# Performance work log

Measured on AMD Instinct MI355X. Metric: run time of the kernel, lower is better.

Reference implementation:

```python
import jax, jax.numpy as jnp
import numpy as np

NUM_CODES = 100000
NUM_EDGES = 20000
DIM = 128
DEG = 32  # nodes per hyperedge -> 640000 incidences


def setup_inputs() -> dict:
    key = jax.random.key(0)
    k1, k2, k3, k4, k5 = jax.random.split(key, 5)
    n_inc = NUM_EDGES * DEG
    # incidence list: edge_ids is sorted (CSR-style), node_ids are member nodes
    node_ids = jax.random.randint(k1, (n_inc,), 0, NUM_CODES, dtype=jnp.int32)
    edge_ids = jnp.repeat(jnp.arange(NUM_EDGES, dtype=jnp.int32), DEG)
    # learned parameters (xavier-ish scales)
    node_emb = jax.random.normal(k2, (NUM_CODES, DIM), jnp.float32) * (1.0 / np.sqrt(DIM))
    edge_emb = jax.random.normal(k3, (NUM_EDGES, DIM), jnp.float32) * (1.0 / np.sqrt(DIM))
    W_e = jax.random.normal(k4, (DIM, DIM), jnp.float32) * (1.0 / np.sqrt(DIM))
    b_e = jnp.zeros((DIM,), jnp.float32)
    W_v = jax.random.normal(k5, (DIM, DIM), jnp.float32) * (1.0 / np.sqrt(DIM))
    b_v = jnp.zeros((DIM,), jnp.float32)
    return {"node_emb": node_emb, "edge_emb": edge_emb, "W_e": W_e, "b_e": b_e,
            "W_v": W_v, "b_v": b_v, "node_ids": node_ids, "edge_ids": edge_ids}


def reference(node_emb, edge_emb, W_e, b_e, W_v, b_v, node_ids, edge_ids):
    N, D = node_emb.shape
    E = edge_emb.shape[0]
    # node -> edge: mean of member node embeddings per hyperedge (segment mean)
    gathered = node_emb[node_ids]                                    # [I, D]
    seg_sum = jax.ops.segment_sum(gathered, edge_ids, num_segments=E)  # [E, D]
    seg_cnt = jax.ops.segment_sum(jnp.ones_like(edge_ids, jnp.float32), edge_ids, num_segments=E)
    mean = seg_sum / jnp.maximum(seg_cnt, 1.0)[:, None]
    # empty edges fall back to their own edge embedding (as in the torch loop)
    edge_ctx = jnp.where(seg_cnt[:, None] > 0, mean, edge_emb)
    edge_ctx = edge_ctx @ W_e.T + b_e                                # lin_e
    # edge -> node: scatter-add edge_ctx back to member nodes
    node_sum = jnp.zeros_like(node_emb).at[node_ids].add(edge_ctx[edge_ids])
    deg = jnp.zeros((N,), jnp.float32).at[node_ids].add(1.0)
    node_cnt = 1.0 + deg  # torch code clamps zeros to 1 BEFORE adding counts
    node_ctx = (node_sum / node_cnt[:, None]) @ W_v.T + b_v          # lin_v
    node_out = node_emb + node_ctx
    edge_out = edge_emb + edge_ctx
    return (node_out, edge_out)
```

## Files before the change

### kernel.cpp

```cpp
#include <hip/hip_runtime.h>

#define DIMS 128
#define DEG 32
#define CAP 32

typedef __attribute__((ext_vector_type(8))) short short8;
typedef __attribute__((ext_vector_type(4))) float floatx4;

static __device__ __forceinline__ unsigned short f2bf(float f) {
  unsigned int u = __float_as_uint(f);
  unsigned int r = (u + 0x7FFFu + ((u >> 16) & 1u)) >> 16;
  return (unsigned short)r;
}
static __device__ __forceinline__ float bf2f(unsigned short v) {
  return __uint_as_float(((unsigned int)v) << 16);
}

__global__ __launch_bounds__(256) void k_cvt_all(
    const float* __restrict__ a0, unsigned short* __restrict__ d0, int n0,
    const float* __restrict__ a1, unsigned short* __restrict__ d1, int n1,
    int* __restrict__ cnt, int ncnt) {
  int t = blockIdx.x * 256 + threadIdx.x;
  if (t < ncnt) cnt[t] = 0;
  int i = t * 4;
  const float* s; unsigned short* d;
  if (i < n0) { s = a0 + i; d = d0 + i; }
  else if (i < n0 + n1) { s = a1 + (i - n0); d = d1 + (i - n0); }
  else return;
  float4 v = *(const float4*)s;
  ushort4 o;
  o.x = f2bf(v.x); o.y = f2bf(v.y); o.z = f2bf(v.z); o.w = f2bf(v.w);
  *(ushort4*)d = o;
}

__global__ __launch_bounds__(256) void k_prep_wc(
    const float* __restrict__ Wv, const float* __restrict__ We,
    const float* __restrict__ be,
    unsigned short* __restrict__ Wc, float* __restrict__ bc) {
  int tid = threadIdx.x;
  if (blockIdx.x == 16) {
    __shared__ float be_s[DIMS];
    if (tid < DIMS) be_s[tid] = be[tid];
    __syncthreads();
    if (tid < DIMS) {
      float s = 0.f;
      for (int c = 0; c < DIMS; ++c) s += Wv[(size_t)tid * DIMS + c] * be_s[c];
      bc[tid] = s;
    }
    return;
  }
  __shared__ __align__(16) float We_s[DIMS][DIMS];
  __shared__ __align__(16) float wv_s[8][DIMS];
  int d0 = blockIdx.x * 8;
#pragma unroll
  for (int u = 0; u < 16; ++u) {
    int idx = tid + u * 256;
    int row = idx >> 5, c4 = idx & 31;
    *(float4*)&We_s[row][c4 * 4] = ((const float4*)We)[idx];
  }
  {
    int row = tid >> 5, c4 = tid & 31;
    *(float4*)&wv_s[row][c4 * 4] = ((const float4*)(Wv + (size_t)d0 * DIMS))[tid];
  }
  __syncthreads();
  int dd = tid >> 5;
  int k4 = (tid & 31) * 4;
  float4 acc = {0.f, 0.f, 0.f, 0.f};
  for (int c = 0; c < DIMS; ++c) {
    float w = wv_s[dd][c];
    float4 we = *(const float4*)&We_s[c][k4];
    acc.x += w * we.x; acc.y += w * we.y; acc.z += w * we.z; acc.w += w * we.w;
  }
  ushort4 o;
  o.x = f2bf(acc.x); o.y = f2bf(acc.y); o.z = f2bf(acc.z); o.w = f2bf(acc.w);
  *(ushort4*)(Wc + (size_t)(d0 + dd) * DIMS + k4) = o;
}

__global__ __launch_bounds__(256) void k_edge_fused(
    const unsigned short* __restrict__ node_emb_bf,
    const int* __restrict__ node_ids,
    const unsigned short* __restrict__ We,
    const unsigned short* __restrict__ Wc,
    const float* __restrict__ be,
    const float* __restrict__ bc,
    const float* __restrict__ edge_emb,
    float* __restrict__ edge_out,
    unsigned short* __restrict__ ectx2,
    int* __restrict__ cnt,
    unsigned short* __restrict__ bucket,
    int E) {
  int e0 = blockIdx.x * 16;
  int tid = threadIdx.x;
  __shared__ int ids[16][DEG];
  __shared__ __align__(16) unsigned short xs[16 * DIMS];
#pragma unroll
  for (int u = 0; u < 2; ++u) {
    int idx = tid + u * 256;
    int ee = idx >> 5, j = idx & 31;
    int e = e0 + ee;
    ids[ee][j] = (e < E) ? node_ids[(size_t)e * DEG + j] : 0;
  }
  __syncthreads();

  {
    int ee = tid >> 4;
    int l8 = tid & 15;
    float acc[8] = {0.f, 0.f, 0.f, 0.f, 0.f, 0.f, 0.f, 0.f};
#pragma unroll
    for (int jb = 0; jb < DEG; jb += 8) {
      short8 v[8];
#pragma unroll
      for (int u = 0; u < 8; ++u) {
        int n = ids[ee][jb + u];
        v[u] = *(const short8*)(node_emb_bf + (size_t)n * DIMS + l8 * 8);
      }
#pragma unroll
      for (int u = 0; u < 8; ++u)
#pragma unroll
        for (int t = 0; t < 8; ++t) acc[t] += bf2f((unsigned short)v[u][t]);
    }
    const float s = 1.0f / (float)DEG;
    short8 o;
#pragma unroll
    for (int t = 0; t < 8; ++t) o[t] = (short)f2bf(acc[t] * s);
    int byt = ee * 256 + ((l8 * 16) ^ ((ee & 7) << 4));
    *(short8*)((char*)xs + byt) = o;
  }

  {
    int ia = tid, ib = tid + 256;
    int ea = e0 + (ia >> 5), eb = e0 + (ib >> 5);
    int na = ids[ia >> 5][ia & 31];
    int nb = ids[ib >> 5][ib & 31];
    int pa = CAP, pb = CAP;
    bool va = ea < E, vb = eb < E;
    if (va) pa = atomicAdd(&cnt[na], 1);
    if (vb) pb = atomicAdd(&cnt[nb], 1);
    if (va && pa < CAP) bucket[(size_t)na * CAP + pa] = (unsigned short)ea;
    if (vb && pb < CAP) bucket[(size_t)nb * CAP + pb] = (unsigned short)eb;
  }
  __syncthreads();

  int wave = tid >> 6;
  int lane = tid & 63;
  int ln = lane & 15;
  int quad = lane >> 4;

  floatx4 acc_e0 = {0.f,0.f,0.f,0.f}, acc_e1 = {0.f,0.f,0.f,0.f};
  floatx4 acc_c0 = {0.f,0.f,0.f,0.f}, acc_c1 = {0.f,0.f,0.f,0.f};

#pragma unroll
  for (int kc = 0; kc < 4; ++kc) {
    int bofs = ln * 256 + ((kc * 64 + quad * 16) ^ ((ln & 7) << 4));
    short8 a = *(const short8*)((const char*)xs + bofs);
    int kb = kc * 32 + quad * 8;
    int wr0 = wave * 32 + ln;
    int wr1 = wave * 32 + 16 + ln;
    short8 bwe0 = *(const short8*)(We + (size_t)wr0 * DIMS + kb);
    short8 bwc0 = *(const short8*)(Wc + (size_t)wr0 * DIMS + kb);
    short8 bwe1 = *(const short8*)(We + (size_t)wr1 * DIMS + kb);
    short8 bwc1 = *(const short8*)(Wc + (size_t)wr1 * DIMS + kb);
    acc_e0 = __builtin_amdgcn_mfma_f32_16x16x32_bf16(bwe0, a, acc_e0, 0, 0, 0);
    acc_c0 = __builtin_amdgcn_mfma_f32_16x16x32_bf16(bwc0, a, acc_c0, 0, 0, 0);
    acc_e1 = __builtin_amdgcn_mfma_f32_16x16x32_bf16(bwe1, a, acc_e1, 0, 0, 0);
    acc_c1 = __builtin_amdgcn_mfma_f32_16x16x32_bf16(bwc1, a, acc_c1, 0, 0, 0);
  }

  int rE = e0 + ln;
  if (rE >= E) return;
#pragma unroll
  for (int t = 0; t < 2; ++t) {
    floatx4 ae = t ? acc_e1 : acc_e0;
    floatx4 ac = t ? acc_c1 : acc_c0;
    int c0 = wave * 32 + t * 16 + quad * 4;
    size_t off = (size_t)rE * DIMS + c0;
    float4 bev = *(const float4*)(be + c0);
    float4 rv = *(const float4*)(edge_emb + off);
    float4 ve;
    ve.x = ae[0] + bev.x + rv.x;
    ve.y = ae[1] + bev.y + rv.y;
    ve.z = ae[2] + bev.z + rv.z;
    ve.w = ae[3] + bev.w + rv.w;
    *(float4*)(edge_out + off) = ve;

    float4 bcv = *(const float4*)(bc + c0);
    ushort4 oc;
    oc.x = f2bf(ac[0] + bcv.x);
    oc.y = f2bf(ac[1] + bcv.y);
    oc.z = f2bf(ac[2] + bcv.z);
    oc.w = f2bf(ac[3] + bcv.w);
    *(ushort4*)(ectx2 + off) = oc;
  }
}

__global__ __launch_bounds__(256) void k_node_out(
    const unsigned short* __restrict__ ectx2,
    const unsigned short* __restrict__ bucket,
    const int* __restrict__ cnt,
    const unsigned short* __restrict__ node_emb_bf,
    const float* __restrict__ bv,
    float* __restrict__ node_out,
    int N) {
  int n0 = blockIdx.x * 16;
  int tid = threadIdx.x;
  __shared__ unsigned short elist[16][CAP];
  __shared__ float scale_s[16];
  __shared__ int cnt_s[16];
  {
    int nn = tid >> 4, p = tid & 15;
    int n = n0 + nn;
    unsigned int v = (n < N)
        ? ((const unsigned int*)(bucket + (size_t)n * CAP))[p] : 0u;
    elist[nn][p * 2] = (unsigned short)(v & 0xFFFFu);
    elist[nn][p * 2 + 1] = (unsigned short)(v >> 16);
  }
  if (tid < 16) {
    int n = n0 + tid;
    int c = (n < N) ? cnt[n] : 0;
    scale_s[tid] = 1.0f / (1.0f + (float)c);
    cnt_s[tid] = c > CAP ? CAP : c;
  }
  __syncthreads();
  int nn = tid >> 4;
  int l8 = tid & 15;
  int n = n0 + nn;
  if (n >= N) return;
  int c = cnt_s[nn];
  float acc[8] = {0.f, 0.f, 0.f, 0.f, 0.f, 0.f, 0.f, 0.f};
  int j = 0;
  for (; j + 4 <= c; j += 4) {
    short8 v0 = *(const short8*)(ectx2 + (size_t)elist[nn][j + 0] * DIMS + l8 * 8);
    short8 v1 = *(const short8*)(ectx2 + (size_t)elist[nn][j + 1] * DIMS + l8 * 8);
    short8 v2 = *(const short8*)(ectx2 + (size_t)elist[nn][j + 2] * DIMS + l8 * 8);
    short8 v3 = *(const short8*)(ectx2 + (size_t)elist[nn][j + 3] * DIMS + l8 * 8);
#pragma unroll
    for (int t = 0; t < 8; ++t)
      acc[t] += bf2f((unsigned short)v0[t]) + bf2f((unsigned short)v1[t]) +
                bf2f((unsigned short)v2[t]) + bf2f((unsigned short)v3[t]);
  }
  for (; j < c; ++j) {
    short8 v = *(const short8*)(ectx2 + (size_t)elist[nn][j] * DIMS + l8 * 8);
#pragma unroll
    for (int t = 0; t < 8; ++t) acc[t] += bf2f((unsigned short)v[t]);
  }
  float sc = scale_s[nn];
  short8 rb = *(const short8*)(node_emb_bf + (size_t)n * DIMS + l8 * 8);
  float4 bv0 = *(const float4*)(bv + l8 * 8);
  float4 bv1 = *(const float4*)(bv + l8 * 8 + 4);
  float4 o0, o1;
  o0.x = acc[0] * sc + bf2f((unsigned short)rb[0]) + bv0.x;
  o0.y = acc[1] * sc + bf2f((unsigned short)rb[1]) + bv0.y;
  o0.z = acc[2] * sc + bf2f((unsigned short)rb[2]) + bv0.z;
  o0.w = acc[3] * sc + bf2f((unsigned short)rb[3]) + bv0.w;
  o1.x = acc[4] * sc + bf2f((unsigned short)rb[4]) + bv1.x;
  o1.y = acc[5] * sc + bf2f((unsigned short)rb[5]) + bv1.y;
  o1.z = acc[6] * sc + bf2f((unsigned short)rb[6]) + bv1.z;
  o1.w = acc[7] * sc + bf2f((unsigned short)rb[7]) + bv1.w;
  float* dst = node_out + (size_t)n * DIMS + l8 * 8;
  *(float4*)dst = o0;
  *(float4*)(dst + 4) = o1;
}

extern "C" void kernel_launch(void* const* d_in, const int* in_sizes, int n_in,
                              void* d_out, int out_size, void* d_ws, size_t ws_size,
                              hipStream_t stream) {
  const float* node_emb = (const float*)d_in[0];
  const float* edge_emb = (const float*)d_in[1];
  const float* W_e      = (const float*)d_in[2];
  const float* b_e      = (const float*)d_in[3];
  const float* W_v      = (const float*)d_in[4];
  const float* b_v      = (const float*)d_in[5];
  const int*   node_ids = (const int*)d_in[6];

  const int N = in_sizes[0] / DIMS;
  const int E = in_sizes[1] / DIMS;

  float* out      = (float*)d_out;
  float* node_out = out;
  float* edge_out = out + (size_t)N * DIMS;

  unsigned short* nb    = (unsigned short*)d_ws;
  unsigned short* ectx2 = nb + (size_t)N * DIMS;
  unsigned short* web   = ectx2 + (size_t)E * DIMS;
  unsigned short* wcb   = web + DIMS * DIMS;
  float* bc  = (float*)(wcb + DIMS * DIMS);
  int* cntb   = (int*)(bc + DIMS);
  unsigned short* bucket = (unsigned short*)(cntb + N);

  int ntot = N * DIMS + DIMS * DIMS;
  k_cvt_all<<<(ntot / 4 + 255) / 256, 256, 0, stream>>>(
      node_emb, nb, N * DIMS, W_e, web, DIMS * DIMS, cntb, N);

  k_prep_wc<<<17, 256, 0, stream>>>(W_v, W_e, b_e, wcb, bc);

  k_edge_fused<<<(E + 15) / 16, 256, 0, stream>>>(
      nb, node_ids, web, wcb, b_e, bc, edge_emb, edge_out, ectx2,
      cntb, bucket, E);

  k_node_out<<<(N + 15) / 16, 256, 0, stream>>>(
      ectx2, bucket, cntb, nb, b_v, node_out, N);
}
```

Baseline: 200.1 us.

## Merge prep kernels and batch node gather loads with zero-row padding

Folds the bf16 conversion and the Wc/bc weight-precompute kernels into one launch, with the weight blocks reading W_e from global memory instead of staging it in a 64KB shared tile. In the node output kernel, the residual and bias loads move ahead of the barrier, and the first eight incident edge rows are loaded unconditionally. Missing entries point at a zeroed extra row appended to ectx2, so these gathers can be in flight together. The aim is to cut one launch and to hide gather latency, at the cost of wasted loads for low-degree nodes and extra workspace for the zero row.

```diff
diff --git a/kernel.cpp b/kernel.cpp
--- a/kernel.cpp
+++ b/kernel.cpp
@@ -16,64 +16,62 @@
   return __uint_as_float(((unsigned int)v) << 16);
 }
 
-__global__ __launch_bounds__(256) void k_cvt_all(
-    const float* __restrict__ a0, unsigned short* __restrict__ d0, int n0,
-    const float* __restrict__ a1, unsigned short* __restrict__ d1, int n1,
-    int* __restrict__ cnt, int ncnt) {
-  int t = blockIdx.x * 256 + threadIdx.x;
+__global__ __launch_bounds__(256) void k_prep(
+    const float* __restrict__ node_emb, unsigned short* __restrict__ nb, int n0,
+    const float* __restrict__ We_f, unsigned short* __restrict__ web, int n1,
+    const float* __restrict__ Wv, const float* __restrict__ be,
+    unsigned short* __restrict__ Wc, float* __restrict__ bc,
+    int* __restrict__ cnt, int ncnt,
+    unsigned short* __restrict__ zrow) {
+  int b = blockIdx.x;
+  int tid = threadIdx.x;
+  if (b < 16) {
+    __shared__ __align__(16) float wv_s[8][DIMS];
+    int d0 = b * 8;
+    {
+      int row = tid >> 5, c4 = tid & 31;
+      *(float4*)&wv_s[row][c4 * 4] = ((const float4*)(Wv + (size_t)d0 * DIMS))[tid];
+    }
+    __syncthreads();
+    int dd = tid >> 5;
+    int k4 = (tid & 31) * 4;
+    float4 acc = {0.f, 0.f, 0.f, 0.f};
+    for (int c = 0; c < DIMS; ++c) {
+      float w = wv_s[dd][c];
+      float4 we = *(const float4*)(We_f + (size_t)c * DIMS + k4);
+      acc.x += w * we.x; acc.y += w * we.y; acc.z += w * we.z; acc.w += w * we.w;
+    }
+    ushort4 o;
+    o.x = f2bf(acc.x); o.y = f2bf(acc.y); o.z = f2bf(acc.z); o.w = f2bf(acc.w);
+    *(ushort4*)(Wc + (size_t)(d0 + dd) * DIMS + k4) = o;
+    return;
+  }
+  if (b == 16) {
+    __shared__ float be_s[DIMS];
+    if (tid < DIMS) be_s[tid] = be[tid];
+    if (tid >= 128 && tid < 144) {
+      short8 z = {0, 0, 0, 0, 0, 0, 0, 0};
+      *(short8*)(zrow + (size_t)(tid - 128) * 8) = z;
+    }
+    __syncthreads();
+    if (tid < DIMS) {
+      float s = 0.f;
+      for (int c = 0; c < DIMS; ++c) s += Wv[(size_t)tid * DIMS + c] * be_s[c];
+      bc[tid] = s;
+    }
+    return;
+  }
+  int t = (b - 17) * 256 + tid;
   if (t < ncnt) cnt[t] = 0;
   int i = t * 4;
   const float* s; unsigned short* d;
-  if (i < n0) { s = a0 + i; d = d0 + i; }
-  else if (i < n0 + n1) { s = a1 + (i - n0); d = d1 + (i - n0); }
+  if (i < n0) { s = node_emb + i; d = nb + i; }
+  else if (i < n0 + n1) { s = We_f + (i - n0); d = web + (i - n0); }
   else return;
   float4 v = *(const float4*)s;
   ushort4 o;
   o.x = f2bf(v.x); o.y = f2bf(v.y); o.z = f2bf(v.z); o.w = f2bf(v.w);
   *(ushort4*)d = o;
-}
-
-__global__ __launch_bounds__(256) void k_prep_wc(
-    const float* __restrict__ Wv, const float* __restrict__ We,
-    const float* __restrict__ be,
-    unsigned short* __restrict__ Wc, float* __restrict__ bc) {
-  int tid = threadIdx.x;
-  if (blockIdx.x == 16) {
-    __shared__ float be_s[DIMS];
-    if (tid < DIMS) be_s[tid] = be[tid];
-    __syncthreads();
-    if (tid < DIMS) {
-      float s = 0.f;
-      for (int c = 0; c < DIMS; ++c) s += Wv[(size_t)tid * DIMS + c] * be_s[c];
-      bc[tid] = s;
-    }
-    return;
-  }
-  __shared__ __align__(16) float We_s[DIMS][DIMS];
-  __shared__ __align__(16) float wv_s[8][DIMS];
-  int d0 = blockIdx.x * 8;
-#pragma unroll
-  for (int u = 0; u < 16; ++u) {
-    int idx = tid + u * 256;
-    int row = idx >> 5, c4 = idx & 31;
-    *(float4*)&We_s[row][c4 * 4] = ((const float4*)We)[idx];
-  }
-  {
-    int row = tid >> 5, c4 = tid & 31;
-    *(float4*)&wv_s[row][c4 * 4] = ((const float4*)(Wv + (size_t)d0 * DIMS))[tid];
-  }
-  __syncthreads();
-  int dd = tid >> 5;
-  int k4 = (tid & 31) * 4;
-  float4 acc = {0.f, 0.f, 0.f, 0.f};
-  for (int c = 0; c < DIMS; ++c) {
-    float w = wv_s[dd][c];
-    float4 we = *(const float4*)&We_s[c][k4];
-    acc.x += w * we.x; acc.y += w * we.y; acc.z += w * we.z; acc.w += w * we.w;
-  }
-  ushort4 o;
-  o.x = f2bf(acc.x); o.y = f2bf(acc.y); o.z = f2bf(acc.z); o.w = f2bf(acc.w);
-  *(ushort4*)(Wc + (size_t)(d0 + dd) * DIMS + k4) = o;
 }
 
 __global__ __launch_bounds__(256) void k_edge_fused(
@@ -131,13 +129,13 @@
     int ia = tid, ib = tid + 256;
     int ea = e0 + (ia >> 5), eb = e0 + (ib >> 5);
     int na = ids[ia >> 5][ia & 31];
-    int nb = ids[ib >> 5][ib & 31];
+    int nb_ = ids[ib >> 5][ib & 31];
     int pa = CAP, pb = CAP;
     bool va = ea < E, vb = eb < E;
     if (va) pa = atomicAdd(&cnt[na], 1);
-    if (vb) pb = atomicAdd(&cnt[nb], 1);
+    if (vb) pb = atomicAdd(&cnt[nb_], 1);
     if (va && pa < CAP) bucket[(size_t)na * CAP + pa] = (unsigned short)ea;
-    if (vb && pb < CAP) bucket[(size_t)nb * CAP + pb] = (unsigned short)eb;
+    if (vb && pb < CAP) bucket[(size_t)nb_ * CAP + pb] = (unsigned short)eb;
   }
   __syncthreads();
 
@@ -200,34 +198,50 @@
     const unsigned short* __restrict__ node_emb_bf,
     const float* __restrict__ bv,
     float* __restrict__ node_out,
-    int N) {
+    int N, int E) {
   int n0 = blockIdx.x * 16;
   int tid = threadIdx.x;
+  int nn = tid >> 4;
+  int l8 = tid & 15;
+  int n = n0 + nn;
+  int nc = (n < N) ? n : (N - 1);
+  short8 rb = *(const short8*)(node_emb_bf + (size_t)nc * DIMS + l8 * 8);
+  float4 bv0 = *(const float4*)(bv + l8 * 8);
+  float4 bv1 = *(const float4*)(bv + l8 * 8 + 4);
+
   __shared__ unsigned short elist[16][CAP];
   __shared__ float scale_s[16];
   __shared__ int cnt_s[16];
   {
-    int nn = tid >> 4, p = tid & 15;
-    int n = n0 + nn;
+    int p = tid & 15;
     unsigned int v = (n < N)
         ? ((const unsigned int*)(bucket + (size_t)n * CAP))[p] : 0u;
     elist[nn][p * 2] = (unsigned short)(v & 0xFFFFu);
     elist[nn][p * 2 + 1] = (unsigned short)(v >> 16);
   }
   if (tid < 16) {
-    int n = n0 + tid;
-    int c = (n < N) ? cnt[n] : 0;
+    int nq = n0 + tid;
+    int c = (nq < N) ? cnt[nq] : 0;
     scale_s[tid] = 1.0f / (1.0f + (float)c);
     cnt_s[tid] = c > CAP ? CAP : c;
   }
   __syncthreads();
-  int nn = tid >> 4;
-  int l8 = tid & 15;
-  int n = n0 + nn;
   if (n >= N) return;
   int c = cnt_s[nn];
   float acc[8] = {0.f, 0.f, 0.f, 0.f, 0.f, 0.f, 0.f, 0.f};
-  int j = 0;
+  {
+    short8 v[8];
+#pragma unroll
+    for (int u = 0; u < 8; ++u) {
+      int idx = (u < c) ? (int)elist[nn][u] : E;
+      v[u] = *(const short8*)(ectx2 + (size_t)idx * DIMS + l8 * 8);
+    }
+#pragma unroll
+    for (int u = 0; u < 8; ++u)
+#pragma unroll
+      for (int t = 0; t < 8; ++t) acc[t] += bf2f((unsigned short)v[u][t]);
+  }
+  int j = 8;
   for (; j + 4 <= c; j += 4) {
     short8 v0 = *(const short8*)(ectx2 + (size_t)elist[nn][j + 0] * DIMS + l8 * 8);
     short8 v1 = *(const short8*)(ectx2 + (size_t)elist[nn][j + 1] * DIMS + l8 * 8);
@@ -244,9 +258,6 @@
     for (int t = 0; t < 8; ++t) acc[t] += bf2f((unsigned short)v[t]);
   }
   float sc = scale_s[nn];
-  short8 rb = *(const short8*)(node_emb_bf + (size_t)n * DIMS + l8 * 8);
-  float4 bv0 = *(const float4*)(bv + l8 * 8);
-  float4 bv1 = *(const float4*)(bv + l8 * 8 + 4);
   float4 o0, o1;
   o0.x = acc[0] * sc + bf2f((unsigned short)rb[0]) + bv0.x;
   o0.y = acc[1] * sc + bf2f((unsigned short)rb[1]) + bv0.y;
@@ -281,22 +292,22 @@
 
   unsigned short* nb    = (unsigned short*)d_ws;
   unsigned short* ectx2 = nb + (size_t)N * DIMS;
-  unsigned short* web   = ectx2 + (size_t)E * DIMS;
+  unsigned short* web   = ectx2 + (size_t)(E + 1) * DIMS;
   unsigned short* wcb   = web + DIMS * DIMS;
   float* bc  = (float*)(wcb + DIMS * DIMS);
   int* cntb   = (int*)(bc + DIMS);
   unsigned short* bucket = (unsigned short*)(cntb + N);
 
   int ntot = N * DIMS + DIMS * DIMS;
-  k_cvt_all<<<(ntot / 4 + 255) / 256, 256, 0, stream>>>(
-      node_emb, nb, N * DIMS, W_e, web, DIMS * DIMS, cntb, N);
-
-  k_prep_wc<<<17, 256, 0, stream>>>(W_v, W_e, b_e, wcb, bc);
+  int nblk = 17 + (ntot / 4 + 255) / 256;
+  k_prep<<<nblk, 256, 0, stream>>>(
+      node_emb, nb, N * DIMS, W_e, web, DIMS * DIMS,
+      W_v, b_e, wcb, bc, cntb, N, ectx2 + (size_t)E * DIMS);
 
   k_edge_fused<<<(E + 15) / 16, 256, 0, stream>>>(
       nb, node_ids, web, wcb, b_e, bc, edge_emb, edge_out, ectx2,
       cntb, bucket, E);
 
   k_node_out<<<(N + 15) / 16, 256, 0, stream>>>(
-      ectx2, bucket, cntb, nb, b_v, node_out, N);
-}
+      ectx2, bucket, cntb, nb, b_v, node_out, N, E);
+}
```

Result: faster. 196.0 us, median of 2 (-2.0%).
